# Performance work log

Measured on AMD Instinct MI355X. Metric: run time of the kernel, lower is better.

## Reference

```python
import jax, jax.numpy as jnp
import numpy as np
import math

N = 8192  # base points
M = 8192  # target points
FEAT = 5
DESC = 4
HID = 32


def setup_inputs() -> dict:
    key = jax.random.key(0)
    ks = jax.random.split(key, 16)
    s = lambda fan_in: 1.0 / np.sqrt(fan_in)
    return {
        "base_pos": jax.random.normal(ks[0], (N, 2), jnp.float32),
        "base_feat": jax.random.normal(ks[1], (N, FEAT), jnp.float32),
        "base_desc": jax.random.normal(ks[2], (DESC,), jnp.float32),
        "target_pos": jax.random.normal(ks[3], (M, 2), jnp.float32),
        "target_feat": jax.random.normal(ks[4], (M, FEAT), jnp.float32),
        "target_desc": jax.random.normal(ks[5], (DESC,), jnp.float32),
        # NodeWeightNet MLP params (Linear(5,32) -> ReLU -> Linear(32,1))
        "w1": jax.random.uniform(ks[6], (FEAT, HID), jnp.float32, -s(FEAT), s(FEAT)),
        "b1": jax.random.uniform(ks[7], (HID,), jnp.float32, -s(FEAT), s(FEAT)),
        "w2": jax.random.uniform(ks[8], (HID, 1), jnp.float32, -s(HID), s(HID)),
        "b2": jax.random.uniform(ks[9], (1,), jnp.float32, -s(HID), s(HID)),
        # descriptor gate params (Linear(4,32) -> ReLU -> Linear(32,1))
        "g1": jax.random.uniform(ks[10], (DESC, HID), jnp.float32, -s(DESC), s(DESC)),
        "gb1": jax.random.uniform(ks[11], (HID,), jnp.float32, -s(DESC), s(DESC)),
        "g2": jax.random.uniform(ks[12], (HID, 1), jnp.float32, -s(HID), s(HID)),
        "gb2": jax.random.uniform(ks[13], (1,), jnp.float32, -s(HID), s(HID)),
        "log_sigma": jnp.asarray(math.log(0.1), jnp.float32),
        "log_scale": jnp.zeros((2,), jnp.float32),
        "bias": jnp.zeros((1,), jnp.float32),
    }


def _node_weights(feat, w1, b1, w2, b2):
    logits = jax.nn.relu(feat @ w1 + b1) @ w2 + b2  # [N,1]
    w = jax.nn.softplus(logits) + 1e-6
    return (w / w.sum())[:, 0]  # [N], sums to 1


def _mmd_term(x, wx, y, wy, inv_two_sigma2):
    # weighted sum of Gaussian kernel over all pairs, via sq-dist expansion
    d2 = (
        (x * x).sum(-1)[:, None]
        + (y * y).sum(-1)[None, :]
        - 2.0 * (x @ y.T)
    )
    k = jnp.exp(-d2 * inv_two_sigma2)
    return jnp.einsum("i,ij,j->", wx, k, wy)


def reference(base_pos, base_feat, base_desc, target_pos, target_feat, target_desc,
              w1, b1, w2, b2, g1, gb1, g2, gb2, log_sigma, log_scale, bias):
    scale = jnp.exp(log_scale)
    bp = base_pos * scale
    tp = target_pos * scale
    sigma = jnp.exp(log_sigma)
    bw = _node_weights(base_feat, w1, b1, w2, b2)
    tw = _node_weights(target_feat, w1, b1, w2, b2)
    # center=True: subtract each cloud's weighted mean
    bp = bp - (bw[:, None] * bp).sum(0)
    tp = tp - (tw[:, None] * tp).sum(0)
    inv = 1.0 / (2.0 * sigma * sigma)
    loss = (
        _mmd_term(bp, bw, bp, bw, inv)
        - 2.0 * _mmd_term(bp, bw, tp, tw, inv)
        + _mmd_term(tp, tw, tp, tw, inv)
    )
    diff = jnp.abs(base_desc - target_desc)  # [4]
    gate = jax.nn.softplus(jax.nn.relu(diff @ g1 + gb1) @ g2 + gb2) + 1e-6  # [1]
    return loss * gate.squeeze() + bias.squeeze()
```

## Files before the change

### kernel.cpp

```cpp
#include <hip/hip_runtime.h>
#include <math.h>


#define WK_THREADS 256
#define MMD_THREADS 256
#define I_PT 4
#define IB (MMD_THREADS * I_PT)
#define JB 128

__device__ __forceinline__ float softplusf(float x) {
    return fmaxf(x, 0.0f) + log1pf(expf(-fabsf(x)));
}

__device__ __forceinline__ float fast_exp2(float x) {
#if __has_builtin(__builtin_amdgcn_exp2f)
    return __builtin_amdgcn_exp2f(x);
#else
    return exp2f(x);
#endif
}

__global__ __launch_bounds__(WK_THREADS) void weight_kernel(
    const float* __restrict__ bpos, const float* __restrict__ bfeat,
    const float* __restrict__ tpos, const float* __restrict__ tfeat,
    const float* __restrict__ w1, const float* __restrict__ b1,
    const float* __restrict__ w2, const float* __restrict__ b2,
    const float* __restrict__ log_sigma, const float* __restrict__ log_scale,
    float4* __restrict__ b4, float4* __restrict__ t4,
    float* __restrict__ wpart, int n, int m)
{
    __shared__ float s_w1[160], s_b1[32], s_w2[32];
    int tid = threadIdx.x;
    if (tid < 160) s_w1[tid] = w1[tid];
    if (tid < 32) { s_b1[tid] = b1[tid]; s_w2[tid] = w2[tid]; }
    __syncthreads();

    int idx = blockIdx.x * WK_THREADS + tid;
    int total = n + m;
    float w = 0.f, px = 0.f, py = 0.f;
    int cloud = 0;
    if (idx < total) {
        const float* pos; const float* feat; int i;
        if (idx < n) { pos = bpos; feat = bfeat; i = idx; cloud = 0; }
        else         { pos = tpos; feat = tfeat; i = idx - n; cloud = 1; }
        float sigma = expf(log_sigma[0]);
        float u = 0.8493218003f / sigma;
        float sx = expf(log_scale[0]) * u;
        float sy = expf(log_scale[1]) * u;
        px = pos[2*i]   * sx;
        py = pos[2*i+1] * sy;
        float f0 = feat[5*i], f1 = feat[5*i+1], f2 = feat[5*i+2],
              f3 = feat[5*i+3], f4 = feat[5*i+4];
        float logit = b2[0];
        #pragma unroll
        for (int h = 0; h < 32; ++h) {
            float a = s_b1[h];
            a = fmaf(f0, s_w1[h],      a);
            a = fmaf(f1, s_w1[32+h],   a);
            a = fmaf(f2, s_w1[64+h],   a);
            a = fmaf(f3, s_w1[96+h],   a);
            a = fmaf(f4, s_w1[128+h],  a);
            a = fmaxf(a, 0.f);
            logit = fmaf(a, s_w2[h], logit);
        }
        w = softplusf(logit) + 1e-6f;
        float h_i = -fmaf(px, px, py * py);
        float4 v = make_float4(px, py, h_i, w);
        if (cloud == 0) b4[i] = v; else t4[i] = v;
    }
    float sw = w, swx = w * px, swy = w * py, sw2 = w * w;
    #pragma unroll
    for (int off = 32; off > 0; off >>= 1) {
        sw  += __shfl_down(sw,  off, 64);
        swx += __shfl_down(swx, off, 64);
        swy += __shfl_down(swy, off, 64);
        sw2 += __shfl_down(sw2, off, 64);
    }
    if ((tid & 63) == 0) {
        int wgid = blockIdx.x * (WK_THREADS / 64) + (tid >> 6);
        float* dst = wpart + wgid * 8;
        float z = (idx < total) ? 1.f : 0.f;
        if (cloud == 0) {
            dst[0] = sw * z; dst[1] = swx * z; dst[2] = swy * z; dst[3] = sw2 * z;
            dst[4] = 0.f;    dst[5] = 0.f;     dst[6] = 0.f;     dst[7] = 0.f;
        } else {
            dst[0] = 0.f;    dst[1] = 0.f;     dst[2] = 0.f;     dst[3] = 0.f;
            dst[4] = sw * z; dst[5] = swx * z; dst[6] = swy * z; dst[7] = sw2 * z;
        }
    }
}

__device__ __forceinline__ void reduce_wpart(const float* __restrict__ wpart,
                                             int nslots, float out[8])
{
    __shared__ float lds8[4][8];
    float v[8];
    #pragma unroll
    for (int k = 0; k < 8; ++k) v[k] = 0.f;
    for (int s = threadIdx.x; s < nslots; s += blockDim.x) {
        #pragma unroll
        for (int k = 0; k < 8; ++k) v[k] += wpart[s * 8 + k];
    }
    #pragma unroll
    for (int off = 32; off > 0; off >>= 1) {
        #pragma unroll
        for (int k = 0; k < 8; ++k) v[k] += __shfl_down(v[k], off, 64);
    }
    if ((threadIdx.x & 63) == 0) {
        #pragma unroll
        for (int k = 0; k < 8; ++k) lds8[threadIdx.x >> 6][k] = v[k];
    }
    __syncthreads();
    #pragma unroll
    for (int k = 0; k < 8; ++k)
        out[k] = lds8[0][k] + lds8[1][k] + lds8[2][k] + lds8[3][k];
    __syncthreads();
}

__global__ __launch_bounds__(MMD_THREADS) void mmd_kernel(
    const float4* __restrict__ b4, const float4* __restrict__ t4,
    const float* __restrict__ wpart, int nwslots,
    float* __restrict__ partial, int n, int m, int gx, int gy)
{
    int t = blockIdx.z;
    const float4* X; const float4* Y; int nx, ny;
    if (t == 0)      { X = b4; Y = b4; nx = n; ny = n; }
    else if (t == 1) { X = b4; Y = t4; nx = n; ny = m; }
    else             { X = t4; Y = t4; nx = m; ny = m; }

    int slot = (t * gy + blockIdx.y) * gx + blockIdx.x;
    int ibase = blockIdx.x * IB;
    int j0 = blockIdx.y * JB;
    bool same = (t != 1);
    if (ibase >= nx || j0 >= ny || (same && j0 < ibase)) {
        if (threadIdx.x == 0) partial[slot] = 0.f;
        return;
    }

    float dx0 = 0.f, dy0 = 0.f;
    if (t == 1) {
        float o[8];
        reduce_wpart(wpart, nwslots, o);
        dx0 = o[1] / o[0] - o[5] / o[4];
        dy0 = o[2] / o[0] - o[6] / o[4];
    }

    __shared__ float4 ytile[JB];
    if (threadIdx.x < JB) {
        int jj = j0 + threadIdx.x;
        ytile[threadIdx.x] = (jj < ny) ? Y[jj] : make_float4(0.f, 0.f, 0.f, 0.f);
    }
    __syncthreads();

    float x2[I_PT], y2[I_PT], hi_[I_PT], wi[I_PT], acc[I_PT];
    int ii_[I_PT];
    #pragma unroll
    for (int s = 0; s < I_PT; ++s) {
        int ii = ibase + s * MMD_THREADS + threadIdx.x;
        ii_[s] = ii;
        float4 v = (ii < nx) ? X[ii] : make_float4(0.f, 0.f, 0.f, 0.f);
        float xc = v.x - dx0, yc = v.y - dy0;
        x2[s] = xc + xc;
        y2[s] = yc + yc;
        hi_[s] = -fmaf(xc, xc, yc * yc);
        wi[s] = v.w;
        acc[s] = 0.f;
    }

    int jn = min(JB, ny - j0);
    if (same && j0 < ibase + IB) {
        #pragma unroll 2
        for (int j = 0; j < jn; ++j) {
            float4 q = ytile[j];
            int jj = j0 + j;
            #pragma unroll
            for (int s = 0; s < I_PT; ++s) {
                float u = hi_[s] + q.z;
                u = fmaf(x2[s], q.x, u);
                u = fmaf(y2[s], q.y, u);
                float e = fast_exp2(u);
                float qw = (jj > ii_[s]) ? q.w : 0.f;
                acc[s] = fmaf(qw, e, acc[s]);
            }
        }
    } else {
        #pragma unroll 2
        for (int j = 0; j < jn; ++j) {
            float4 q = ytile[j];
            #pragma unroll
            for (int s = 0; s < I_PT; ++s) {
                float u = hi_[s] + q.z;
                u = fmaf(x2[s], q.x, u);
                u = fmaf(y2[s], q.y, u);
                acc[s] = fmaf(q.w, fast_exp2(u), acc[s]);
            }
        }
    }
    float r = 0.f;
    #pragma unroll
    for (int s = 0; s < I_PT; ++s) r = fmaf(wi[s], acc[s], r);

    #pragma unroll
    for (int off = 32; off > 0; off >>= 1) r += __shfl_down(r, off, 64);
    __shared__ float wsum[MMD_THREADS / 64];
    if ((threadIdx.x & 63) == 0) wsum[threadIdx.x >> 6] = r;
    __syncthreads();
    if (threadIdx.x == 0) {
        float tot = 0.f;
        #pragma unroll
        for (int k = 0; k < MMD_THREADS / 64; ++k) tot += wsum[k];
        partial[slot] = tot;
    }
}

__global__ __launch_bounds__(256) void final_kernel(
    const float* __restrict__ bdesc, const float* __restrict__ tdesc,
    const float* __restrict__ g1, const float* __restrict__ gb1,
    const float* __restrict__ g2, const float* __restrict__ gb2,
    const float* __restrict__ bias, const float* __restrict__ wpart, int nwslots,
    const float* __restrict__ partial, int gx, int gy,
    float* __restrict__ out)
{
    float o[8];
    reduce_wpart(wpart, nwslots, o);
    float sb = o[0], st = o[4];
    float sw2b = o[3], sw2t = o[7];

    int np1 = gx * gy;
    float p0 = 0.f, p1 = 0.f, p2 = 0.f;
    for (int k = threadIdx.x; k < 3 * np1; k += 256) {
        float v = partial[k];
        int term = k / np1;
        if (term == 0) p0 += v; else if (term == 1) p1 += v; else p2 += v;
    }
    #pragma unroll
    for (int off = 32; off > 0; off >>= 1) {
        p0 += __shfl_down(p0, off, 64);
        p1 += __shfl_down(p1, off, 64);
        p2 += __shfl_down(p2, off, 64);
    }
    __shared__ float lds3[4][3];
    if ((threadIdx.x & 63) == 0) {
        lds3[threadIdx.x >> 6][0] = p0;
        lds3[threadIdx.x >> 6][1] = p1;
        lds3[threadIdx.x >> 6][2] = p2;
    }
    __syncthreads();
    float P0 = lds3[0][0] + lds3[1][0] + lds3[2][0] + lds3[3][0];
    float P1 = lds3[0][1] + lds3[1][1] + lds3[2][1] + lds3[3][1];
    float P2 = lds3[0][2] + lds3[1][2] + lds3[2][2] + lds3[3][2];

    float T0 = 2.f * P0 + sw2b;
    float T2 = 2.f * P2 + sw2t;

    float a = 0.f;
    if (threadIdx.x < 32) {
        int h = threadIdx.x;
        float d0 = fabsf(bdesc[0] - tdesc[0]);
        float d1 = fabsf(bdesc[1] - tdesc[1]);
        float d2 = fabsf(bdesc[2] - tdesc[2]);
        float d3 = fabsf(bdesc[3] - tdesc[3]);
        float v = gb1[h];
        v = fmaf(d0, g1[h],      v);
        v = fmaf(d1, g1[32+h],   v);
        v = fmaf(d2, g1[64+h],   v);
        v = fmaf(d3, g1[96+h],   v);
        a = fmaxf(v, 0.f) * g2[h];
    }
    #pragma unroll
    for (int off = 16; off > 0; off >>= 1) a += __shfl_down(a, off, 64);
    if (threadIdx.x == 0) {
        float gate = softplusf(a + gb2[0]) + 1e-6f;
        float loss = T0 / (sb * sb) - 2.f * P1 / (sb * st) + T2 / (st * st);
        out[0] = loss * gate + bias[0];
    }
}

extern "C" void kernel_launch(void* const* d_in, const int* in_sizes, int n_in,
                              void* d_out, int out_size, void* d_ws, size_t ws_size,
                              hipStream_t stream)
{
    const float* bpos      = (const float*)d_in[0];
    const float* bfeat     = (const float*)d_in[1];
    const float* bdesc     = (const float*)d_in[2];
    const float* tpos      = (const float*)d_in[3];
    const float* tfeat     = (const float*)d_in[4];
    const float* tdesc     = (const float*)d_in[5];
    const float* w1        = (const float*)d_in[6];
    const float* b1        = (const float*)d_in[7];
    const float* w2        = (const float*)d_in[8];
    const float* b2        = (const float*)d_in[9];
    const float* g1        = (const float*)d_in[10];
    const float* gb1       = (const float*)d_in[11];
    const float* g2        = (const float*)d_in[12];
    const float* gb2       = (const float*)d_in[13];
    const float* log_sigma = (const float*)d_in[14];
    const float* log_scale = (const float*)d_in[15];
    const float* bias      = (const float*)d_in[16];
    float* out = (float*)d_out;

    int n = in_sizes[0] / 2;
    int m = in_sizes[3] / 2;

    int wb = (n + m + WK_THREADS - 1) / WK_THREADS;
    int nwslots = wb * (WK_THREADS / 64);
    int nmax = n > m ? n : m;
    int gx = (nmax + IB - 1) / IB;
    int gy = (nmax + JB - 1) / JB;

    char* ws = (char*)d_ws;
    float4* b4    = (float4*)ws;
    float4* t4    = (float4*)(ws + (size_t)n * sizeof(float4));
    float* wpart  = (float*)(ws + (size_t)(n + m) * sizeof(float4));
    float* partial = wpart + (size_t)nwslots * 8;

    weight_kernel<<<wb, WK_THREADS, 0, stream>>>(
        bpos, bfeat, tpos, tfeat, w1, b1, w2, b2, log_sigma, log_scale,
        b4, t4, wpart, n, m);

    dim3 grid(gx, gy, 3);
    mmd_kernel<<<grid, MMD_THREADS, 0, stream>>>(
        b4, t4, wpart, nwslots, partial, n, m, gx, gy);

    final_kernel<<<1, 256, 0, stream>>>(
        bdesc, tdesc, g1, gb1, g2, gb2, bias, wpart, nwslots,
        partial, gx, gy, out);
}
```

Measured before the change: 126.0 us.

## Fuse final reduction into MMD kernel and use packed FP32 math in inner loop

The final reduction kernel is folded into the MMD kernel through a last-block-done atomic ticket counter, which is reset in the weight kernel, so one kernel launch is removed. The y tile is stored as structure-of-arrays in shared memory so two j points can be processed at once. The non-diagonal inner loop uses v_pk_add/v_pk_fma packed FP32 instructions via inline asm, which halves the VALU instruction count for distance and accumulation, while exp2 stays scalar. The cost is threadfence and atomic overhead in every block, plus a serial tail reduction in the last block.

```diff
diff --git a/kernel.cpp b/kernel.cpp
--- a/kernel.cpp
+++ b/kernel.cpp
@@ -7,6 +7,8 @@
 #define I_PT 4
 #define IB (MMD_THREADS * I_PT)
 #define JB 128
+
+typedef float f32x2 __attribute__((ext_vector_type(2)));
 
 __device__ __forceinline__ float softplusf(float x) {
     return fmaxf(x, 0.0f) + log1pf(expf(-fabsf(x)));
@@ -27,12 +29,13 @@
     const float* __restrict__ w2, const float* __restrict__ b2,
     const float* __restrict__ log_sigma, const float* __restrict__ log_scale,
     float4* __restrict__ b4, float4* __restrict__ t4,
-    float* __restrict__ wpart, int n, int m)
+    float* __restrict__ wpart, unsigned* __restrict__ counter, int n, int m)
 {
     __shared__ float s_w1[160], s_b1[32], s_w2[32];
     int tid = threadIdx.x;
     if (tid < 160) s_w1[tid] = w1[tid];
     if (tid < 32) { s_b1[tid] = b1[tid]; s_w2[tid] = w2[tid]; }
+    if (blockIdx.x == 0 && tid == 0) counter[0] = 0u;
     __syncthreads();
 
     int idx = blockIdx.x * WK_THREADS + tid;
@@ -120,7 +123,12 @@
 __global__ __launch_bounds__(MMD_THREADS) void mmd_kernel(
     const float4* __restrict__ b4, const float4* __restrict__ t4,
     const float* __restrict__ wpart, int nwslots,
-    float* __restrict__ partial, int n, int m, int gx, int gy)
+    float* __restrict__ partial, unsigned* __restrict__ counter,
+    int n, int m, int gx, int gy, int ngrid,
+    const float* __restrict__ bdesc, const float* __restrict__ tdesc,
+    const float* __restrict__ g1, const float* __restrict__ gb1,
+    const float* __restrict__ g2, const float* __restrict__ gb2,
+    const float* __restrict__ bias, float* __restrict__ out)
 {
     int t = blockIdx.z;
     const float4* X; const float4* Y; int nx, ny;
@@ -132,73 +140,96 @@
     int ibase = blockIdx.x * IB;
     int j0 = blockIdx.y * JB;
     bool same = (t != 1);
-    if (ibase >= nx || j0 >= ny || (same && j0 < ibase)) {
-        if (threadIdx.x == 0) partial[slot] = 0.f;
-        return;
-    }
-
-    float dx0 = 0.f, dy0 = 0.f;
-    if (t == 1) {
-        float o[8];
-        reduce_wpart(wpart, nwslots, o);
-        dx0 = o[1] / o[0] - o[5] / o[4];
-        dy0 = o[2] / o[0] - o[6] / o[4];
-    }
-
-    __shared__ float4 ytile[JB];
-    if (threadIdx.x < JB) {
-        int jj = j0 + threadIdx.x;
-        ytile[threadIdx.x] = (jj < ny) ? Y[jj] : make_float4(0.f, 0.f, 0.f, 0.f);
-    }
-    __syncthreads();
-
-    float x2[I_PT], y2[I_PT], hi_[I_PT], wi[I_PT], acc[I_PT];
-    int ii_[I_PT];
-    #pragma unroll
-    for (int s = 0; s < I_PT; ++s) {
-        int ii = ibase + s * MMD_THREADS + threadIdx.x;
-        ii_[s] = ii;
-        float4 v = (ii < nx) ? X[ii] : make_float4(0.f, 0.f, 0.f, 0.f);
-        float xc = v.x - dx0, yc = v.y - dy0;
-        x2[s] = xc + xc;
-        y2[s] = yc + yc;
-        hi_[s] = -fmaf(xc, xc, yc * yc);
-        wi[s] = v.w;
-        acc[s] = 0.f;
-    }
-
-    int jn = min(JB, ny - j0);
-    if (same && j0 < ibase + IB) {
-        #pragma unroll 2
-        for (int j = 0; j < jn; ++j) {
-            float4 q = ytile[j];
-            int jj = j0 + j;
-            #pragma unroll
-            for (int s = 0; s < I_PT; ++s) {
-                float u = hi_[s] + q.z;
-                u = fmaf(x2[s], q.x, u);
-                u = fmaf(y2[s], q.y, u);
-                float e = fast_exp2(u);
-                float qw = (jj > ii_[s]) ? q.w : 0.f;
-                acc[s] = fmaf(qw, e, acc[s]);
+    bool active = (ibase < nx) && (j0 < ny) && !(same && j0 < ibase);
+
+    __shared__ float sx[JB], sy[JB], sz[JB], sw_[JB];
+
+    float r = 0.f;
+    if (active) {
+        float dx0 = 0.f, dy0 = 0.f;
+        if (t == 1) {
+            float o[8];
+            reduce_wpart(wpart, nwslots, o);
+            dx0 = o[1] / o[0] - o[5] / o[4];
+            dy0 = o[2] / o[0] - o[6] / o[4];
+        }
+
+        if (threadIdx.x < JB) {
+            int jj = j0 + threadIdx.x;
+            float4 v = (jj < ny) ? Y[jj] : make_float4(0.f, 0.f, 0.f, 0.f);
+            sx[threadIdx.x] = v.x; sy[threadIdx.x] = v.y;
+            sz[threadIdx.x] = v.z; sw_[threadIdx.x] = v.w;
+        }
+        __syncthreads();
+
+        f32x2 x22[I_PT], y22[I_PT], h2[I_PT], acc2[I_PT];
+        float wi[I_PT]; int ii_[I_PT];
+        #pragma unroll
+        for (int s = 0; s < I_PT; ++s) {
+            int ii = ibase + s * MMD_THREADS + threadIdx.x;
+            ii_[s] = ii;
+            float4 v = (ii < nx) ? X[ii] : make_float4(0.f, 0.f, 0.f, 0.f);
+            float xc = v.x - dx0, yc = v.y - dy0;
+            float hx = -fmaf(xc, xc, yc * yc);
+            x22[s] = (f32x2){xc + xc, xc + xc};
+            y22[s] = (f32x2){yc + yc, yc + yc};
+            h2[s]  = (f32x2){hx, hx};
+            wi[s] = v.w;
+            acc2[s] = (f32x2){0.f, 0.f};
+        }
+
+        int jn = min(JB, ny - j0);
+        if (same && j0 < ibase + IB) {
+            for (int j = 0; j < jn; ++j) {
+                float qx = sx[j], qy = sy[j], qz = sz[j], qw = sw_[j];
+                int jj = j0 + j;
+                #pragma unroll
+                for (int s = 0; s < I_PT; ++s) {
+                    float u = h2[s].x + qz;
+                    u = fmaf(x22[s].x, qx, u);
+                    u = fmaf(y22[s].x, qy, u);
+                    float e = fast_exp2(u);
+                    float qwm = (jj > ii_[s]) ? qw : 0.f;
+                    acc2[s].x = fmaf(qwm, e, acc2[s].x);
+                }
             }
-        }
-    } else {
-        #pragma unroll 2
-        for (int j = 0; j < jn; ++j) {
-            float4 q = ytile[j];
-            #pragma unroll
-            for (int s = 0; s < I_PT; ++s) {
-                float u = hi_[s] + q.z;
-                u = fmaf(x2[s], q.x, u);
-                u = fmaf(y2[s], q.y, u);
-                acc[s] = fmaf(q.w, fast_exp2(u), acc[s]);
+        } else {
+            const f32x2* px = (const f32x2*)sx;
+            const f32x2* py = (const f32x2*)sy;
+            const f32x2* pz = (const f32x2*)sz;
+            const f32x2* pw = (const f32x2*)sw_;
+            int jn2 = jn >> 1;
+            #pragma unroll 2
+            for (int j2 = 0; j2 < jn2; ++j2) {
+                f32x2 qx = px[j2], qy = py[j2], qz = pz[j2], qw = pw[j2];
+                #pragma unroll
+                for (int s = 0; s < I_PT; ++s) {
+                    f32x2 u;
+                    asm("v_pk_add_f32 %0, %1, %2" : "=v"(u) : "v"(h2[s]), "v"(qz));
+                    asm("v_pk_fma_f32 %0, %1, %2, %0" : "+v"(u) : "v"(x22[s]), "v"(qx));
+                    asm("v_pk_fma_f32 %0, %1, %2, %0" : "+v"(u) : "v"(y22[s]), "v"(qy));
+                    f32x2 e;
+                    e.x = fast_exp2(u.x);
+                    e.y = fast_exp2(u.y);
+                    asm("v_pk_fma_f32 %0, %1, %2, %0" : "+v"(acc2[s]) : "v"(qw), "v"(e));
+                }
             }
-        }
-    }
-    float r = 0.f;
-    #pragma unroll
-    for (int s = 0; s < I_PT; ++s) r = fmaf(wi[s], acc[s], r);
+            if (jn & 1) {
+                int j = jn - 1;
+                float qx = sx[j], qy = sy[j], qz = sz[j], qw = sw_[j];
+                #pragma unroll
+                for (int s = 0; s < I_PT; ++s) {
+                    float u = h2[s].x + qz;
+                    u = fmaf(x22[s].x, qx, u);
+                    u = fmaf(y22[s].x, qy, u);
+                    acc2[s].x = fmaf(qw, fast_exp2(u), acc2[s].x);
+                }
+            }
+        }
+        #pragma unroll
+        for (int s = 0; s < I_PT; ++s)
+            r = fmaf(wi[s], acc2[s].x + acc2[s].y, r);
+    }
 
     #pragma unroll
     for (int off = 32; off > 0; off >>= 1) r += __shfl_down(r, off, 64);
@@ -211,16 +242,14 @@
         for (int k = 0; k < MMD_THREADS / 64; ++k) tot += wsum[k];
         partial[slot] = tot;
     }
-}
-
-__global__ __launch_bounds__(256) void final_kernel(
-    const float* __restrict__ bdesc, const float* __restrict__ tdesc,
-    const float* __restrict__ g1, const float* __restrict__ gb1,
-    const float* __restrict__ g2, const float* __restrict__ gb2,
-    const float* __restrict__ bias, const float* __restrict__ wpart, int nwslots,
-    const float* __restrict__ partial, int gx, int gy,
-    float* __restrict__ out)
-{
+
+    __threadfence();
+    __shared__ unsigned ticket;
+    if (threadIdx.x == 0) ticket = atomicAdd(counter, 1u);
+    __syncthreads();
+    if (ticket != (unsigned)(ngrid - 1)) return;
+    __threadfence();
+
     float o[8];
     reduce_wpart(wpart, nwslots, o);
     float sb = o[0], st = o[4];
@@ -228,7 +257,7 @@
 
     int np1 = gx * gy;
     float p0 = 0.f, p1 = 0.f, p2 = 0.f;
-    for (int k = threadIdx.x; k < 3 * np1; k += 256) {
+    for (int k = threadIdx.x; k < 3 * np1; k += MMD_THREADS) {
         float v = partial[k];
         int term = k / np1;
         if (term == 0) p0 += v; else if (term == 1) p1 += v; else p2 += v;
@@ -307,22 +336,21 @@
     int nmax = n > m ? n : m;
     int gx = (nmax + IB - 1) / IB;
     int gy = (nmax + JB - 1) / JB;
+    int ngrid = gx * gy * 3;
 
     char* ws = (char*)d_ws;
     float4* b4    = (float4*)ws;
     float4* t4    = (float4*)(ws + (size_t)n * sizeof(float4));
     float* wpart  = (float*)(ws + (size_t)(n + m) * sizeof(float4));
     float* partial = wpart + (size_t)nwslots * 8;
+    unsigned* counter = (unsigned*)(partial + (size_t)ngrid);
 
     weight_kernel<<<wb, WK_THREADS, 0, stream>>>(
         bpos, bfeat, tpos, tfeat, w1, b1, w2, b2, log_sigma, log_scale,
-        b4, t4, wpart, n, m);
+        b4, t4, wpart, counter, n, m);
 
     dim3 grid(gx, gy, 3);
     mmd_kernel<<<grid, MMD_THREADS, 0, stream>>>(
-        b4, t4, wpart, nwslots, partial, n, m, gx, gy);
-
-    final_kernel<<<1, 256, 0, stream>>>(
-        bdesc, tdesc, g1, gb1, g2, gb2, bias, wpart, nwslots,
-        partial, gx, gy, out);
-}
+        b4, t4, wpart, nwslots, partial, counter, n, m, gx, gy, ngrid,
+        bdesc, tdesc, g1, gb1, g2, gb2, bias, out);
+}
```

Measured after the change: 214.2 us. 1.7x slower.
